# Optimization experiments

Hardware: AMD Instinct MI355X
Metric: run time of the kernel (lower is better)

## Reference

```python
import jax, jax.numpy as jnp
import numpy as np

D = 512  # input_size
H = 512  # hidden_size
N = 64   # batch
T = 512  # timesteps


def setup_inputs() -> dict:
    key = jax.random.key(0)
    k1, k2, k3, k4 = jax.random.split(key, 4)
    x = jax.random.normal(k1, (N, T, D), dtype=jnp.float32)
    h0 = jax.random.normal(k2, (N, H), dtype=jnp.float32)
    Wx = jax.random.normal(k3, (D, H), dtype=jnp.float32) / np.sqrt(D)
    Wh = jax.random.normal(k4, (H, H), dtype=jnp.float32) / np.sqrt(H)
    b = jnp.zeros((H,), dtype=jnp.float32)
    return {"x": x, "h0": h0, "Wx": Wx, "Wh": Wh, "b": b}


def reference(x, h0, Wx, Wh, b):
    # Precompute input projections for all timesteps in one big GEMM:
    # same math as per-step x_t @ Wx inside the loop.
    xWx = jnp.einsum('ntd,dh->nth', x, Wx) + b  # (N, T, H)

    def step(prev_h, xwx_t):
        next_h = jnp.tanh(prev_h @ Wh + xwx_t)  # (N, H)
        return next_h, next_h

    # scan over time: xWx transposed to (T, N, H)
    _, hs = jax.lax.scan(step, h0, jnp.swapaxes(xWx, 0, 1))
    return jnp.swapaxes(hs, 0, 1)  # (N, T, H)
```

## Files before the change

### kernel.cpp

```cpp
#include <hip/hip_runtime.h>
#include <hip/hip_bf16.h>

#define NB 64
#define TT 512
#define HH 512
#define DD 512

typedef __attribute__((ext_vector_type(8))) __bf16 bf16x8;
typedef __attribute__((ext_vector_type(4))) float f32x4;

__device__ __forceinline__ unsigned short f2bf_rn(float f) {
    union { float f; unsigned u; } v; v.f = f;
    unsigned r = v.u + 0x7FFFu + ((v.u >> 16) & 1u);
    return (unsigned short)(r >> 16);
}
__device__ __forceinline__ float bf2f(unsigned short s) {
    union { unsigned u; float f; } v; v.u = ((unsigned)s) << 16;
    return v.f;
}

__global__ __launch_bounds__(256) void wt_kernel(const float* __restrict__ Wx,
                                                 unsigned short* __restrict__ Wt) {
    const int bk = blockIdx.x >> 3, bn = blockIdx.x & 7;
    const int k0 = bk * 64, n0 = bn * 64;
    __shared__ float tile[64][65];
    const int t = threadIdx.x;
    const int kr = t >> 2, seg = t & 3;
    const float4* src = (const float4*)&Wx[(k0 + kr) * HH + n0 + seg * 16];
    float4 a = src[0], b = src[1], c = src[2], d = src[3];
    float vv[16];
    *(float4*)&vv[0] = a; *(float4*)&vv[4] = b; *(float4*)&vv[8] = c; *(float4*)&vv[12] = d;
#pragma unroll
    for (int q = 0; q < 16; ++q) tile[kr][seg * 16 + q] = vv[q];
    __syncthreads();
    const int nr = t >> 2;
    unsigned hu[8], lu[8];
#pragma unroll
    for (int i = 0; i < 8; ++i) {
        float f0 = tile[seg * 16 + 2 * i + 0][nr];
        float f1 = tile[seg * 16 + 2 * i + 1][nr];
        unsigned short h0 = f2bf_rn(f0); unsigned short l0 = f2bf_rn(f0 - bf2f(h0));
        unsigned short h1 = f2bf_rn(f1); unsigned short l1 = f2bf_rn(f1 - bf2f(h1));
        hu[i] = (unsigned)h0 | ((unsigned)h1 << 16);
        lu[i] = (unsigned)l0 | ((unsigned)l1 << 16);
    }
    unsigned short* dh = &Wt[(n0 + nr) * 1024 + k0 + seg * 16];
    unsigned short* dl = dh + 512;
    ((uint4*)dh)[0] = make_uint4(hu[0], hu[1], hu[2], hu[3]);
    ((uint4*)dh)[1] = make_uint4(hu[4], hu[5], hu[6], hu[7]);
    ((uint4*)dl)[0] = make_uint4(lu[0], lu[1], lu[2], lu[3]);
    ((uint4*)dl)[1] = make_uint4(lu[4], lu[5], lu[6], lu[7]);
}

#define LDA 72
__global__ __launch_bounds__(256) void proj_kernel(const float* __restrict__ x,
                                                   const unsigned short* __restrict__ Wt,
                                                   const float* __restrict__ bias,
                                                   float* __restrict__ out) {
    __shared__ __align__(16) unsigned short a_hi[64 * LDA];
    __shared__ __align__(16) unsigned short a_lo[64 * LDA];
    __shared__ __align__(16) unsigned short b_hi[64 * LDA];
    __shared__ __align__(16) unsigned short b_lo[64 * LDA];

    const int bx = blockIdx.x;
    const int i0 = (bx >> 3) * 64;
    const int n0 = (bx & 7) * 64;
    const int t = threadIdx.x;
    const int row = t >> 2, seg = t & 3;
    const int lane = t & 63, wid = t >> 6;
    const int wm = (wid >> 1) * 32, wn = (wid & 1) * 32;
    const int fr = lane & 15;

    f32x4 acc00 = {0.f, 0.f, 0.f, 0.f}, acc01 = acc00, acc10 = acc00, acc11 = acc00;

    for (int kc = 0; kc < 8; ++kc) {
        __syncthreads();
        {
            const float4* src = (const float4*)&x[(i0 + row) * DD + kc * 64 + seg * 16];
            float4 a = src[0], b = src[1], c = src[2], d = src[3];
            float vv[16];
            *(float4*)&vv[0] = a; *(float4*)&vv[4] = b; *(float4*)&vv[8] = c; *(float4*)&vv[12] = d;
            unsigned hu[8], lu[8];
#pragma unroll
            for (int i = 0; i < 8; ++i) {
                unsigned short h0 = f2bf_rn(vv[2 * i]); unsigned short l0 = f2bf_rn(vv[2 * i] - bf2f(h0));
                unsigned short h1 = f2bf_rn(vv[2 * i + 1]); unsigned short l1 = f2bf_rn(vv[2 * i + 1] - bf2f(h1));
                hu[i] = (unsigned)h0 | ((unsigned)h1 << 16);
                lu[i] = (unsigned)l0 | ((unsigned)l1 << 16);
            }
            uint4* dh = (uint4*)&a_hi[row * LDA + seg * 16];
            uint4* dl = (uint4*)&a_lo[row * LDA + seg * 16];
            dh[0] = make_uint4(hu[0], hu[1], hu[2], hu[3]);
            dh[1] = make_uint4(hu[4], hu[5], hu[6], hu[7]);
            dl[0] = make_uint4(lu[0], lu[1], lu[2], lu[3]);
            dl[1] = make_uint4(lu[4], lu[5], lu[6], lu[7]);
        }
        {
            const uint4* sh = (const uint4*)&Wt[(n0 + row) * 1024 + kc * 64 + seg * 16];
            const uint4* sl = (const uint4*)&Wt[(n0 + row) * 1024 + 512 + kc * 64 + seg * 16];
            uint4 h0v = sh[0], h1v = sh[1], l0v = sl[0], l1v = sl[1];
            uint4* dh = (uint4*)&b_hi[row * LDA + seg * 16];
            uint4* dl = (uint4*)&b_lo[row * LDA + seg * 16];
            dh[0] = h0v; dh[1] = h1v; dl[0] = l0v; dl[1] = l1v;
        }
        __syncthreads();
#pragma unroll
        for (int s = 0; s < 2; ++s) {
            const int ko = s * 32 + (lane >> 4) * 8;
            bf16x8 ah0 = *(const bf16x8*)&a_hi[(wm + fr) * LDA + ko];
            bf16x8 ah1 = *(const bf16x8*)&a_hi[(wm + 16 + fr) * LDA + ko];
            bf16x8 al0 = *(const bf16x8*)&a_lo[(wm + fr) * LDA + ko];
            bf16x8 al1 = *(const bf16x8*)&a_lo[(wm + 16 + fr) * LDA + ko];
            bf16x8 bh0 = *(const bf16x8*)&b_hi[(wn + fr) * LDA + ko];
            bf16x8 bh1 = *(const bf16x8*)&b_hi[(wn + 16 + fr) * LDA + ko];
            bf16x8 bl0 = *(const bf16x8*)&b_lo[(wn + fr) * LDA + ko];
            bf16x8 bl1 = *(const bf16x8*)&b_lo[(wn + 16 + fr) * LDA + ko];
            acc00 = __builtin_amdgcn_mfma_f32_16x16x32_bf16(ah0, bh0, acc00, 0, 0, 0);
            acc00 = __builtin_amdgcn_mfma_f32_16x16x32_bf16(ah0, bl0, acc00, 0, 0, 0);
            acc00 = __builtin_amdgcn_mfma_f32_16x16x32_bf16(al0, bh0, acc00, 0, 0, 0);
            acc01 = __builtin_amdgcn_mfma_f32_16x16x32_bf16(ah0, bh1, acc01, 0, 0, 0);
            acc01 = __builtin_amdgcn_mfma_f32_16x16x32_bf16(ah0, bl1, acc01, 0, 0, 0);
            acc01 = __builtin_amdgcn_mfma_f32_16x16x32_bf16(al0, bh1, acc01, 0, 0, 0);
            acc10 = __builtin_amdgcn_mfma_f32_16x16x32_bf16(ah1, bh0, acc10, 0, 0, 0);
            acc10 = __builtin_amdgcn_mfma_f32_16x16x32_bf16(ah1, bl0, acc10, 0, 0, 0);
            acc10 = __builtin_amdgcn_mfma_f32_16x16x32_bf16(al1, bh0, acc10, 0, 0, 0);
            acc11 = __builtin_amdgcn_mfma_f32_16x16x32_bf16(ah1, bh1, acc11, 0, 0, 0);
            acc11 = __builtin_amdgcn_mfma_f32_16x16x32_bf16(ah1, bl1, acc11, 0, 0, 0);
            acc11 = __builtin_amdgcn_mfma_f32_16x16x32_bf16(al1, bh1, acc11, 0, 0, 0);
        }
    }
    const float bc0 = bias[n0 + wn + fr];
    const float bc1 = bias[n0 + wn + 16 + fr];
#pragma unroll
    for (int r = 0; r < 4; ++r) {
        int rw0 = i0 + wm + (lane >> 4) * 4 + r;
        int rw1 = rw0 + 16;
        out[rw0 * HH + n0 + wn + fr]      = acc00[r] + bc0;
        out[rw0 * HH + n0 + wn + 16 + fr] = acc01[r] + bc1;
        out[rw1 * HH + n0 + wn + fr]      = acc10[r] + bc0;
        out[rw1 * HH + n0 + wn + 16 + fr] = acc11[r] + bc1;
    }
}

__global__ __launch_bounds__(512, 2) void rec_kernel(const float* __restrict__ h0,
                                                     const float* __restrict__ Wh,
                                                     float* __restrict__ out,
                                                     unsigned long long* __restrict__ pbuf) {
    const int b = blockIdx.x;
    const int g = b & 63;
    const int s = b >> 6;
    const int tid = threadIdx.x;
    const int c = tid & 127;
    const int kg = tid >> 7;
    const bool fin = (kg == s);
    const int jf = c + 128 * s;

    float w[4][32];
#pragma unroll
    for (int r = 0; r < 32; ++r) {
        const float* row = &Wh[(s * 128 + kg * 32 + r) * HH + c];
#pragma unroll
        for (int cc = 0; cc < 4; ++cc) w[cc][r] = row[128 * cc];
    }

    __shared__ float hsl[2][128];
    __shared__ float red[4][128];
    if (tid < 128) hsl[0][tid] = h0[g * HH + s * 128 + tid];

    float xw = fin ? out[(g * TT + 0) * HH + jf] : 0.f;
    __syncthreads();

#pragma unroll 1
    for (int t = 0; t < TT; ++t) {
        const int slot = t & 1;
        const unsigned tg = (unsigned)(t + 1);
        const unsigned mbase = ((unsigned)slot * NB + (unsigned)g) * 12u;

        const float4* h4 = (const float4*)&hsl[slot][kg * 32];
        float4 hv[8];
#pragma unroll
        for (int r4 = 0; r4 < 8; ++r4) hv[r4] = h4[r4];

#pragma unroll
        for (int cc = 0; cc < 4; ++cc) {
            float a0 = 0.f, a1 = 0.f, a2 = 0.f, a3 = 0.f;
#pragma unroll
            for (int r4 = 0; r4 < 8; ++r4) {
                float4 h = hv[r4];
                a0 = fmaf(w[cc][4 * r4 + 0], h.x, a0);
                a1 = fmaf(w[cc][4 * r4 + 1], h.y, a1);
                a2 = fmaf(w[cc][4 * r4 + 2], h.z, a2);
                a3 = fmaf(w[cc][4 * r4 + 3], h.w, a3);
            }
            float p = (a0 + a1) + (a2 + a3);
            if (cc == s) {
                red[kg][c] = p;
            } else {
                const int sidx = s - (s > cc ? 1 : 0);
                const unsigned plane = (unsigned)(sidx * 4 + kg);
                unsigned long long pv = ((unsigned long long)tg << 32) |
                                        (unsigned long long)__float_as_uint(p);
                __hip_atomic_store(&pbuf[(mbase + plane) * HH + (unsigned)(c + 128 * cc)],
                                   pv, __ATOMIC_RELAXED, __HIP_MEMORY_SCOPE_AGENT);
            }
        }
        __syncthreads();

        if (fin) {
            float xwn = (t + 1 < TT) ? out[(g * TT + t + 1) * HH + jf] : 0.f;
            const unsigned long long* A = &pbuf[mbase * HH + (unsigned)jf];
            unsigned long long v[12];
            bool ok;
            do {
                ok = true;
#pragma unroll
                for (int i = 0; i < 12; ++i)
                    v[i] = __hip_atomic_load(A + (unsigned)i * HH,
                                             __ATOMIC_RELAXED, __HIP_MEMORY_SCOPE_AGENT);
#pragma unroll
                for (int i = 0; i < 12; ++i)
                    ok = ok && ((unsigned)(v[i] >> 32) == tg);
            } while (!ok);
            float sum = (red[0][c] + red[1][c]) + (red[2][c] + red[3][c]) + xw;
#pragma unroll
            for (int i = 0; i < 12; ++i)
                sum += __uint_as_float((unsigned)v[i]);
            float hn = 1.f - 2.f / (__expf(2.f * sum) + 1.f);
            out[(g * TT + t) * HH + jf] = hn;
            hsl[slot ^ 1][c] = hn;
            xw = xwn;
        }
        __syncthreads();
    }
}

extern "C" void kernel_launch(void* const* d_in, const int* in_sizes, int n_in,
                              void* d_out, int out_size, void* d_ws, size_t ws_size,
                              hipStream_t stream) {
    (void)in_sizes; (void)n_in; (void)out_size; (void)ws_size;
    const float* x  = (const float*)d_in[0];
    const float* h0 = (const float*)d_in[1];
    const float* Wx = (const float*)d_in[2];
    const float* Wh = (const float*)d_in[3];
    const float* bv = (const float*)d_in[4];
    float* out = (float*)d_out;

    const size_t PBUF_BYTES = 2ull * NB * 12 * HH * sizeof(unsigned long long);
    unsigned long long* pbuf = (unsigned long long*)d_ws;
    unsigned short* Wt = (unsigned short*)((char*)d_ws + PBUF_BYTES);

    hipMemsetAsync(pbuf, 0, PBUF_BYTES, stream);

    wt_kernel<<<64, 256, 0, stream>>>(Wx, Wt);

    proj_kernel<<<(32768 / 64) * (HH / 64), 256, 0, stream>>>(x, Wt, bv, out);

    rec_kernel<<<NB * 4, 512, 0, stream>>>(h0, Wh, out, pbuf);
}
```

Measured before the change: 960.0 us.

## Reduce k-partials in-wave via shuffles, cutting cross-block partial exchange fourfold

New measurement: 897.6 us. -6.5%, faster.

```diff
diff --git a/kernel.cpp b/kernel.cpp
--- a/kernel.cpp
+++ b/kernel.cpp
@@ -150,22 +150,24 @@
     const int g = b & 63;
     const int s = b >> 6;
     const int tid = threadIdx.x;
-    const int c = tid & 127;
-    const int kg = tid >> 7;
-    const bool fin = (kg == s);
-    const int jf = c + 128 * s;
+    const int wave = tid >> 6, lane = tid & 63;
+    const int kg = lane >> 4;
+    const int li = lane & 15;
+    const int cidx = wave * 16 + li;
+    const bool fin = (kg == 0);
+    const int jf = cidx + 128 * s;
+    const int ccq = fin ? s : ((kg - 1) + ((kg - 1) >= s ? 1 : 0));
 
     float w[4][32];
 #pragma unroll
     for (int r = 0; r < 32; ++r) {
-        const float* row = &Wh[(s * 128 + kg * 32 + r) * HH + c];
+        const float* row = &Wh[(s * 128 + kg * 32 + r) * HH + cidx];
 #pragma unroll
         for (int cc = 0; cc < 4; ++cc) w[cc][r] = row[128 * cc];
     }
 
-    __shared__ float hsl[2][128];
-    __shared__ float red[4][128];
-    if (tid < 128) hsl[0][tid] = h0[g * HH + s * 128 + tid];
+    __shared__ float hpart[2][4 * 36];
+    if (tid < 128) hpart[0][(tid >> 5) * 36 + (tid & 31)] = h0[g * HH + s * 128 + tid];
 
     float xw = fin ? out[(g * TT + 0) * HH + jf] : 0.f;
     __syncthreads();
@@ -174,13 +176,14 @@
     for (int t = 0; t < TT; ++t) {
         const int slot = t & 1;
         const unsigned tg = (unsigned)(t + 1);
-        const unsigned mbase = ((unsigned)slot * NB + (unsigned)g) * 12u;
-
-        const float4* h4 = (const float4*)&hsl[slot][kg * 32];
+        const unsigned mbase = ((unsigned)slot * NB + (unsigned)g) * 3u;
+
         float4 hv[8];
+        const float4* h4 = (const float4*)&hpart[slot][kg * 36];
 #pragma unroll
         for (int r4 = 0; r4 < 8; ++r4) hv[r4] = h4[r4];
 
+        float p[4];
 #pragma unroll
         for (int cc = 0; cc < 4; ++cc) {
             float a0 = 0.f, a1 = 0.f, a2 = 0.f, a3 = 0.f;
@@ -192,42 +195,37 @@
                 a2 = fmaf(w[cc][4 * r4 + 2], h.z, a2);
                 a3 = fmaf(w[cc][4 * r4 + 3], h.w, a3);
             }
-            float p = (a0 + a1) + (a2 + a3);
-            if (cc == s) {
-                red[kg][c] = p;
-            } else {
-                const int sidx = s - (s > cc ? 1 : 0);
-                const unsigned plane = (unsigned)(sidx * 4 + kg);
-                unsigned long long pv = ((unsigned long long)tg << 32) |
-                                        (unsigned long long)__float_as_uint(p);
-                __hip_atomic_store(&pbuf[(mbase + plane) * HH + (unsigned)(c + 128 * cc)],
-                                   pv, __ATOMIC_RELAXED, __HIP_MEMORY_SCOPE_AGENT);
-            }
-        }
-        __syncthreads();
-
-        if (fin) {
+            p[cc] = (a0 + a1) + (a2 + a3);
+        }
+#pragma unroll
+        for (int cc = 0; cc < 4; ++cc) {
+            p[cc] += __shfl_xor(p[cc], 16, 64);
+            p[cc] += __shfl_xor(p[cc], 32, 64);
+        }
+
+        if (!fin) {
+            const int sidx = s - (s > ccq ? 1 : 0);
+            unsigned long long pv = ((unsigned long long)tg << 32) |
+                                    (unsigned long long)__float_as_uint(p[ccq]);
+            __hip_atomic_store(&pbuf[(mbase + (unsigned)sidx) * HH + (unsigned)(cidx + 128 * ccq)],
+                               pv, __ATOMIC_RELAXED, __HIP_MEMORY_SCOPE_AGENT);
+        } else {
             float xwn = (t + 1 < TT) ? out[(g * TT + t + 1) * HH + jf] : 0.f;
-            const unsigned long long* A = &pbuf[mbase * HH + (unsigned)jf];
-            unsigned long long v[12];
-            bool ok;
+            const unsigned long long* a0p = &pbuf[mbase * HH + (unsigned)jf];
+            const unsigned long long* a1p = a0p + HH;
+            const unsigned long long* a2p = a1p + HH;
+            unsigned long long v0, v1, v2;
             do {
-                ok = true;
-#pragma unroll
-                for (int i = 0; i < 12; ++i)
-                    v[i] = __hip_atomic_load(A + (unsigned)i * HH,
-                                             __ATOMIC_RELAXED, __HIP_MEMORY_SCOPE_AGENT);
-#pragma unroll
-                for (int i = 0; i < 12; ++i)
-                    ok = ok && ((unsigned)(v[i] >> 32) == tg);
-            } while (!ok);
-            float sum = (red[0][c] + red[1][c]) + (red[2][c] + red[3][c]) + xw;
-#pragma unroll
-            for (int i = 0; i < 12; ++i)
-                sum += __uint_as_float((unsigned)v[i]);
+                v0 = __hip_atomic_load(a0p, __ATOMIC_RELAXED, __HIP_MEMORY_SCOPE_AGENT);
+                v1 = __hip_atomic_load(a1p, __ATOMIC_RELAXED, __HIP_MEMORY_SCOPE_AGENT);
+                v2 = __hip_atomic_load(a2p, __ATOMIC_RELAXED, __HIP_MEMORY_SCOPE_AGENT);
+            } while ((unsigned)(v0 >> 32) != tg || (unsigned)(v1 >> 32) != tg ||
+                     (unsigned)(v2 >> 32) != tg);
+            float sum = p[s] + __uint_as_float((unsigned)v0) + __uint_as_float((unsigned)v1) +
+                        __uint_as_float((unsigned)v2) + xw;
             float hn = 1.f - 2.f / (__expf(2.f * sum) + 1.f);
             out[(g * TT + t) * HH + jf] = hn;
-            hsl[slot ^ 1][c] = hn;
+            hpart[slot ^ 1][(cidx >> 5) * 36 + (cidx & 31)] = hn;
             xw = xwn;
         }
         __syncthreads();
@@ -245,7 +243,7 @@
     const float* bv = (const float*)d_in[4];
     float* out = (float*)d_out;
 
-    const size_t PBUF_BYTES = 2ull * NB * 12 * HH * sizeof(unsigned long long);
+    const size_t PBUF_BYTES = 2ull * NB * 3 * HH * sizeof(unsigned long long);
     unsigned long long* pbuf = (unsigned long long*)d_ws;
     unsigned short* Wt = (unsigned short*)((char*)d_ws + PBUF_BYTES);
 
```
